# Optimization experiments

Measured on AMD Instinct MI355X. Metric: run time of the kernel, lower is better.

The kernel has to match this reference:

```python
import jax, jax.numpy as jnp
import numpy as np
from jax import lax

GAMMA = 0.001  # init kwarg gamma
DN = ('NCHW', 'OIHW', 'NCHW')


def _maxpool2(x):
    # 2x2 max pool, stride 2, NCHW
    return lax.reduce_window(x, -jnp.inf, lax.max, (1, 1, 2, 2), (1, 1, 2, 2), 'VALID')


def _features(x, w1, b1, w2, b2):
    h = lax.conv_general_dilated(x, w1, (1, 1), 'SAME', dimension_numbers=DN)
    h = _maxpool2(jax.nn.relu(h + b1[None, :, None, None]))
    h = lax.conv_general_dilated(h, w2, (1, 1), 'SAME', dimension_numbers=DN)
    h = _maxpool2(jax.nn.relu(h + b2[None, :, None, None]))
    return h.reshape(h.shape[0], -1)  # [N, 16*7*7=784]


def setup_inputs() -> dict:
    key = jax.random.key(0)
    ks = jax.random.split(key, 7)
    x = jax.random.normal(ks[0], (4096, 1, 28, 28), dtype=jnp.float32)
    w1 = jax.random.normal(ks[1], (8, 1, 3, 3), dtype=jnp.float32) * 0.1
    b1 = jax.random.normal(ks[2], (8,), dtype=jnp.float32) * 0.1
    w2 = jax.random.normal(ks[3], (16, 8, 3, 3), dtype=jnp.float32) * 0.1
    b2 = jax.random.normal(ks[4], (16,), dtype=jnp.float32) * 0.1
    support = jax.random.uniform(ks[5], (8192, 784), dtype=jnp.float32)
    alpha = jax.random.normal(ks[6], (8192, 4), dtype=jnp.float32)
    return {'x': x, 'w1': w1, 'b1': b1, 'w2': w2, 'b2': b2,
            'support': support, 'alpha': alpha}


def reference(x, w1, b1, w2, b2, support, alpha):
    feats = _features(x, w1, b1, w2, b2)                      # [N, 784]
    # Pairwise squared distances via expansion (replaces the N*M python loop)
    f2 = jnp.sum(feats * feats, axis=1, keepdims=True)        # [N, 1]
    s2 = jnp.sum(support * support, axis=1)[None, :]          # [1, M]
    d2 = f2 + s2 - 2.0 * (feats @ support.T)                  # [N, M]
    K = jnp.exp(-GAMMA * d2)                                  # RBF kernel matrix
    return K @ alpha                                          # [N, n_classes]
```

## Files before the change

kernel.cpp:

```cpp
#include <hip/hip_runtime.h>
#include <hip/hip_bf16.h>
#include <cstdint>

#define GAMMA 0.001f
#define TILE_BYTES 114688

typedef __attribute__((ext_vector_type(4))) float f32x4;
typedef __attribute__((ext_vector_type(8))) int v8i;
typedef __attribute__((ext_vector_type(8))) short bh8;
typedef unsigned char u8;

__device__ inline unsigned pack4_fp8(float4 f) {
  unsigned p = __builtin_amdgcn_cvt_pk_fp8_f32(f.x, f.y, 0, false);
  p = __builtin_amdgcn_cvt_pk_fp8_f32(f.z, f.w, p, true);
  return p;
}

__device__ inline ushort bf16u(float v) {
  __hip_bfloat16 h = __float2bfloat16(v);
  return *(ushort*)&h;
}

__global__ __launch_bounds__(256, 4) void conv_prep_kernel(
    const float* __restrict__ x, const float* __restrict__ w1,
    const float* __restrict__ b1, const float* __restrict__ w2,
    const float* __restrict__ b2, const float* __restrict__ support,
    const float* __restrict__ alpha, u8* __restrict__ feats_t,
    u8* __restrict__ sup_t, float* __restrict__ beta,
    float* __restrict__ ef) {
  int tid = threadIdx.x;
  int bx = blockIdx.x;

  if (bx >= 2048) {
    int lane = tid & 63, wave = tid >> 6;
    int m = (bx - 2048) * 4 + wave;
    const float* row = support + (size_t)m * 784;
    int mt = m >> 7, mr = m & 127;
    u8* tb = sup_t + (size_t)mt * TILE_BYTES;
    float ss = 0.f;
    if (lane < 56) {
      uint4 w;
      if (lane < 49) {
        float4 f0 = ((const float4*)row)[lane * 4 + 0];
        float4 f1 = ((const float4*)row)[lane * 4 + 1];
        float4 f2 = ((const float4*)row)[lane * 4 + 2];
        float4 f3 = ((const float4*)row)[lane * 4 + 3];
        ss = f0.x * f0.x + f0.y * f0.y + f0.z * f0.z + f0.w * f0.w +
             f1.x * f1.x + f1.y * f1.y + f1.z * f1.z + f1.w * f1.w +
             f2.x * f2.x + f2.y * f2.y + f2.z * f2.z + f2.w * f2.w +
             f3.x * f3.x + f3.y * f3.y + f3.z * f3.z + f3.w * f3.w;
        w.x = pack4_fp8(f0); w.y = pack4_fp8(f1);
        w.z = pack4_fp8(f2); w.w = pack4_fp8(f3);
      } else {
        w.x = 0; w.y = 0; w.z = 0; w.w = 0;
      }
      int kk = lane >> 3, u = lane & 7, q = u >> 1, h = u & 1;
      int qs = q ^ ((mr >> 1) & 3);
      *(uint4*)(tb + kk * 16384 + h * 8192 + mr * 64 + qs * 16) = w;
    }
#pragma unroll
    for (int s = 1; s < 64; s <<= 1) ss += __shfl_xor(ss, s, 64);
    if (lane == 0) {
      float es = __expf(-GAMMA * ss);
      float4 a = ((const float4*)alpha)[m];
      float4 b;
      b.x = es * a.x; b.y = es * a.y; b.z = es * a.z; b.w = es * a.w;
      ((float4*)beta)[m] = b;
    }
    return;
  }

  __shared__ float xp[2][900];
  __shared__ alignas(16) ushort a1h[2][2048];
  __shared__ float w1s[72], b1s[8], b2s[16];
  __shared__ float w2s[1152];
  __shared__ alignas(8) ushort sc[2][16][212];
  __shared__ alignas(16) u8 fb[2][784];
  __shared__ float red[256];

  int lane = tid & 63, wave = tid >> 6;

  for (int t = tid; t < 1800; t += 256) ((float*)xp)[t] = 0.f;
  for (int t = tid; t < 1024; t += 256) ((uint4*)a1h)[t] = (uint4){0, 0, 0, 0};
  if (tid < 72) w1s[tid] = w1[tid];
  if (tid < 8) b1s[tid] = b1[tid];
  if (tid < 16) b2s[tid] = b2[tid];
  for (int t = tid; t < 1152; t += 256) w2s[t] = w2[t];
  __syncthreads();

  int oc = lane & 15, quad = lane >> 4;
  bh8 wf[3];
#pragma unroll
  for (int g = 0; g < 3; g++) {
    int tap = g * 4 + quad;
#pragma unroll
    for (int j = 0; j < 8; j++) {
      float v = (tap < 9) ? w2s[oc * 72 + j * 9 + tap] : 0.f;
      wf[g][j] = (short)bf16u(v);
    }
  }

  for (int t = tid; t < 392; t += 256) {
    int img = t >= 196, j = t - img * 196;
    float4 v = ((const float4*)(x + (size_t)(bx * 2 + img) * 784))[j];
    int r = j / 7, c = (j % 7) * 4;
    float* p = &xp[img][(r + 1) * 30 + (c + 1)];
    p[0] = v.x; p[1] = v.y; p[2] = v.z; p[3] = v.w;
  }
  __syncthreads();

  for (int idx = tid; idx < 3136; idx += 256) {
    int img = idx >= 1568;
    int rem = idx - img * 1568;
    int c = rem / 196, r2 = rem % 196;
    int ph = r2 / 14, pw = r2 % 14;
    const float* w = &w1s[c * 9];
    const float* xb = &xp[img][(2 * ph) * 30 + (2 * pw)];
    float t[4][4];
#pragma unroll
    for (int a = 0; a < 4; a++) {
      float2 u0 = *(const float2*)(xb + a * 30);
      float2 u1 = *(const float2*)(xb + a * 30 + 2);
      t[a][0] = u0.x; t[a][1] = u0.y; t[a][2] = u1.x; t[a][3] = u1.y;
    }
    float s00 = 0, s01 = 0, s10 = 0, s11 = 0;
#pragma unroll
    for (int dy = 0; dy < 3; dy++)
#pragma unroll
      for (int dx = 0; dx < 3; dx++) {
        float wv = w[dy * 3 + dx];
        s00 += t[dy][dx] * wv;     s01 += t[dy][dx + 1] * wv;
        s10 += t[dy + 1][dx] * wv; s11 += t[dy + 1][dx + 1] * wv;
      }
    float mx = fmaxf(fmaxf(s00, s01), fmaxf(s10, s11));
    float val = fmaxf(mx + b1s[c], 0.f);
    a1h[img][((ph + 1) * 16 + (pw + 1)) * 8 + c] = bf16u(val);
  }
  __syncthreads();

  {
    int img2 = wave >> 1, half = wave & 1;
    int Tstart = half * 7, Tcnt = half ? 6 : 7;
    const ushort* abase = a1h[img2];
    int mrow = lane & 15;
    for (int t = 0; t < Tcnt; ++t) {
      int T = Tstart + t;
      int p = T * 16 + mrow;
      int pc = p > 195 ? 195 : p;
      int y = pc / 14, xq = pc - y * 14;
      int cell = y * 16 + xq;
      f32x4 acc = (f32x4){0, 0, 0, 0};
#pragma unroll
      for (int g = 0; g < 3; g++) {
        int tap = g * 4 + quad;
        const ushort* ap;
        if (g == 2 && quad > 0) {
          ap = abase;
        } else {
          int dy = tap / 3, dx = tap - dy * 3;
          ap = abase + (cell + dy * 16 + dx) * 8;
        }
        bh8 af = *(const bh8*)ap;
        acc = __builtin_amdgcn_mfma_f32_16x16x32_bf16(af, wf[g], acc, 0, 0, 0);
      }
      int pos0 = T * 16 + quad * 4;
      ushort4 s4;
      s4.x = bf16u(acc.x); s4.y = bf16u(acc.y);
      s4.z = bf16u(acc.z); s4.w = bf16u(acc.w);
      *(ushort4*)(&sc[img2][oc][pos0]) = s4;
    }
  }
  __syncthreads();

  int img = tid >> 7, r = tid & 127;
  float fsq = 0.f;
  if (r < 112) {
    int o = r & 15, y7 = r >> 4;
    const ushort* srow = sc[img][o];
    float bo = b2s[o];
#pragma unroll
    for (int x7 = 0; x7 < 7; x7++) {
      int p = 28 * y7 + 2 * x7;
      unsigned u0 = *(const unsigned*)(&srow[p]);
      unsigned u1 = *(const unsigned*)(&srow[p + 14]);
      float a = __uint_as_float(u0 << 16);
      float b = __uint_as_float(u0 & 0xffff0000u);
      float c = __uint_as_float(u1 << 16);
      float d = __uint_as_float(u1 & 0xffff0000u);
      float mx = fmaxf(fmaxf(a, b), fmaxf(c, d));
      float val = fmaxf(mx + bo, 0.f);
      fb[img][o * 49 + y7 * 7 + x7] =
          (u8)(__builtin_amdgcn_cvt_pk_fp8_f32(val, 0.f, 0, false) & 0xff);
      fsq += val * val;
    }
  }
  red[tid] = fsq;
  __syncthreads();
  for (int s = 64; s > 0; s >>= 1) {
    if ((tid & 127) < s) red[tid] += red[tid + s];
    __syncthreads();
  }
  if ((tid & 127) == 0) ef[bx * 2 + img] = __expf(-GAMMA * red[tid]);

  if (tid < 112) {
    int im = tid >= 56, j = tid - im * 56;
    uint4 v;
    if (j < 49) v = ((const uint4*)fb[im])[j];
    else { v.x = 0; v.y = 0; v.z = 0; v.w = 0; }
    int n = bx * 2 + im;
    int nt = n >> 7, nr = n & 127;
    int kk = j >> 3, u = j & 7, q = u >> 1, h = u & 1;
    int qs = q ^ ((nr >> 1) & 3);
    *(uint4*)(feats_t + (size_t)nt * TILE_BYTES + kk * 16384 + h * 8192 +
              nr * 64 + qs * 16) = v;
  }
}

__global__ __launch_bounds__(256, 2) void rbf_gemm_kernel(
    const u8* __restrict__ feats_t, const u8* __restrict__ sup_t,
    const float* __restrict__ beta, float* __restrict__ partial) {
  __shared__ alignas(16) u8 As[16384];
  __shared__ alignas(16) u8 Bs[16384];
  int tid = threadIdx.x;
  int wave = tid >> 6, lane = tid & 63;
  int bx = blockIdx.x;
  int chunk = bx & 63, nb = bx >> 6;
  const u8* at = feats_t + (size_t)nb * TILE_BYTES;
  const u8* bt = sup_t + (size_t)chunk * TILE_BYTES;
  int wn = wave >> 1, wm = wave & 1;
  int col = lane & 15, quad = lane >> 4;
  int slot = quad ^ ((col >> 1) & 3);

  f32x4 acc[4][4];
#pragma unroll
  for (int i = 0; i < 4; i++)
#pragma unroll
    for (int j = 0; j < 4; j++) acc[i][j] = (f32x4){0, 0, 0, 0};

  for (int kk = 0; kk < 7; ++kk) {
    const u8* ak = at + kk * 16384 + tid * 16;
    const u8* bk = bt + kk * 16384 + tid * 16;
    u8* la = As + tid * 16;
    u8* lb = Bs + tid * 16;
#pragma unroll
    for (int s = 0; s < 4; s++) {
      __builtin_amdgcn_global_load_lds(
          (const __attribute__((address_space(1))) void*)(ak + s * 4096),
          (__attribute__((address_space(3))) void*)(la + s * 4096), 16, 0, 0);
      __builtin_amdgcn_global_load_lds(
          (const __attribute__((address_space(1))) void*)(bk + s * 4096),
          (__attribute__((address_space(3))) void*)(lb + s * 4096), 16, 0, 0);
    }
    __syncthreads();
    v8i av[4], bv[4];
#pragma unroll
    for (int i = 0; i < 4; i++) {
      const u8* p = As + (wn * 64 + i * 16 + col) * 64 + slot * 16;
      int4 lo = *(const int4*)p;
      int4 hi = *(const int4*)(p + 8192);
      av[i] = (v8i){lo.x, lo.y, lo.z, lo.w, hi.x, hi.y, hi.z, hi.w};
    }
#pragma unroll
    for (int j = 0; j < 4; j++) {
      const u8* p = Bs + (wm * 64 + j * 16 + col) * 64 + slot * 16;
      int4 lo = *(const int4*)p;
      int4 hi = *(const int4*)(p + 8192);
      bv[j] = (v8i){lo.x, lo.y, lo.z, lo.w, hi.x, hi.y, hi.z, hi.w};
    }
#pragma unroll
    for (int i = 0; i < 4; i++)
#pragma unroll
      for (int j = 0; j < 4; j++)
        acc[i][j] = __builtin_amdgcn_mfma_scale_f32_16x16x128_f8f6f4(
            av[i], bv[j], acc[i][j], 0, 0, 0, 0x7f7f7f7f, 0, 0x7f7f7f7f);
    __syncthreads();
  }

#pragma unroll
  for (int i = 0; i < 4; i++)
#pragma unroll
    for (int j = 0; j < 4; j++) {
      acc[i][j].x = __expf(2.f * GAMMA * acc[i][j].x);
      acc[i][j].y = __expf(2.f * GAMMA * acc[i][j].y);
      acc[i][j].z = __expf(2.f * GAMMA * acc[i][j].z);
      acc[i][j].w = __expf(2.f * GAMMA * acc[i][j].w);
    }
  int n0 = nb * 128, m0 = chunk * 128;
#pragma unroll
  for (int c = 0; c < 4; ++c) {
    float bl[4];
#pragma unroll
    for (int j = 0; j < 4; j++)
      bl[j] = beta[(m0 + wm * 64 + j * 16 + col) * 4 + c];
#pragma unroll
    for (int i = 0; i < 4; i++) {
      f32x4 s = acc[i][0] * bl[0] + acc[i][1] * bl[1] + acc[i][2] * bl[2] +
                acc[i][3] * bl[3];
#pragma unroll
      for (int st = 1; st < 16; st <<= 1) {
        s.x += __shfl_xor(s.x, st, 16);
        s.y += __shfl_xor(s.y, st, 16);
        s.z += __shfl_xor(s.z, st, 16);
        s.w += __shfl_xor(s.w, st, 16);
      }
      if (col == c) {
        int n = n0 + wn * 64 + i * 16 + quad * 4;
        float* pp = partial + (((size_t)chunk * 2 + wm) * 4096 + n) * 4 + c;
        pp[0] = s.x; pp[4] = s.y; pp[8] = s.z; pp[12] = s.w;
      }
    }
  }
}

__global__ __launch_bounds__(256) void reduce_kernel(
    const float* __restrict__ partial, const float* __restrict__ ef,
    float* __restrict__ out) {
  __shared__ float4 sred[4][64];
  int nl = threadIdx.x & 63, chq = threadIdx.x >> 6;
  int n = blockIdx.x * 64 + nl;
  const float4* p = (const float4*)partial;
  float sx = 0, sy = 0, sz = 0, sw = 0;
  for (int ch = chq * 32; ch < chq * 32 + 32; ch++) {
    float4 v = p[(size_t)ch * 4096 + n];
    sx += v.x; sy += v.y; sz += v.z; sw += v.w;
  }
  sred[chq][nl] = (float4){sx, sy, sz, sw};
  __syncthreads();
  if (chq == 0) {
    float4 a = sred[0][nl], b = sred[1][nl], c = sred[2][nl], d = sred[3][nl];
    float e = ef[n];
    float4 o;
    o.x = e * (a.x + b.x + c.x + d.x);
    o.y = e * (a.y + b.y + c.y + d.y);
    o.z = e * (a.z + b.z + c.z + d.z);
    o.w = e * (a.w + b.w + c.w + d.w);
    ((float4*)out)[n] = o;
  }
}

extern "C" void kernel_launch(void* const* d_in, const int* in_sizes, int n_in,
                              void* d_out, int out_size, void* d_ws,
                              size_t ws_size, hipStream_t stream) {
  const float* x = (const float*)d_in[0];
  const float* w1 = (const float*)d_in[1];
  const float* b1 = (const float*)d_in[2];
  const float* w2 = (const float*)d_in[3];
  const float* b2 = (const float*)d_in[4];
  const float* support = (const float*)d_in[5];
  const float* alpha = (const float*)d_in[6];
  float* out = (float*)d_out;

  u8* ws = (u8*)d_ws;
  u8* sup_t = ws;
  u8* feats_t = ws + 7340032;
  float* beta = (float*)(ws + 11010048);
  float* ef = (float*)(ws + 11141120);
  float* partial = (float*)(ws + 11157504);

  conv_prep_kernel<<<4096, 256, 0, stream>>>(x, w1, b1, w2, b2, support, alpha,
                                             feats_t, sup_t, beta, ef);
  rbf_gemm_kernel<<<2048, 256, 0, stream>>>(feats_t, sup_t, beta, partial);
  reduce_kernel<<<64, 256, 0, stream>>>(partial, ef, out);
}
```

Baseline: 167.8 us.

## Load GEMM operand fragments directly from global memory, dropping LDS staging

The RBF GEMM kernel no longer stages A and B tiles through shared memory with global_load_lds and barriers. Each wave now reads its MFMA fragments directly from the pre-swizzled global layout into registers, and the k-loop is unrolled by two. This removes the LDS round trip and both __syncthreads per iteration. In exchange, two waves sharing a tile each load the same data from global memory, so the kernel leans on L2/L1 hits and more register-held loads are in flight.

```diff
diff --git a/kernel.cpp b/kernel.cpp
--- a/kernel.cpp
+++ b/kernel.cpp
@@ -219,50 +219,40 @@
 __global__ __launch_bounds__(256, 2) void rbf_gemm_kernel(
     const u8* __restrict__ feats_t, const u8* __restrict__ sup_t,
     const float* __restrict__ beta, float* __restrict__ partial) {
-  __shared__ alignas(16) u8 As[16384];
-  __shared__ alignas(16) u8 Bs[16384];
   int tid = threadIdx.x;
   int wave = tid >> 6, lane = tid & 63;
   int bx = blockIdx.x;
   int chunk = bx & 63, nb = bx >> 6;
-  const u8* at = feats_t + (size_t)nb * TILE_BYTES;
-  const u8* bt = sup_t + (size_t)chunk * TILE_BYTES;
   int wn = wave >> 1, wm = wave & 1;
   int col = lane & 15, quad = lane >> 4;
   int slot = quad ^ ((col >> 1) & 3);
 
+  const u8* abase = feats_t + (size_t)nb * TILE_BYTES +
+                    (wn * 64 + col) * 64 + slot * 16;
+  const u8* bbase = sup_t + (size_t)chunk * TILE_BYTES +
+                    (wm * 64 + col) * 64 + slot * 16;
+
   f32x4 acc[4][4];
 #pragma unroll
   for (int i = 0; i < 4; i++)
 #pragma unroll
     for (int j = 0; j < 4; j++) acc[i][j] = (f32x4){0, 0, 0, 0};
 
+#pragma unroll 2
   for (int kk = 0; kk < 7; ++kk) {
-    const u8* ak = at + kk * 16384 + tid * 16;
-    const u8* bk = bt + kk * 16384 + tid * 16;
-    u8* la = As + tid * 16;
-    u8* lb = Bs + tid * 16;
-#pragma unroll
-    for (int s = 0; s < 4; s++) {
-      __builtin_amdgcn_global_load_lds(
-          (const __attribute__((address_space(1))) void*)(ak + s * 4096),
-          (__attribute__((address_space(3))) void*)(la + s * 4096), 16, 0, 0);
-      __builtin_amdgcn_global_load_lds(
-          (const __attribute__((address_space(1))) void*)(bk + s * 4096),
-          (__attribute__((address_space(3))) void*)(lb + s * 4096), 16, 0, 0);
-    }
-    __syncthreads();
+    const u8* ak = abase + kk * 16384;
+    const u8* bk = bbase + kk * 16384;
     v8i av[4], bv[4];
 #pragma unroll
     for (int i = 0; i < 4; i++) {
-      const u8* p = As + (wn * 64 + i * 16 + col) * 64 + slot * 16;
+      const u8* p = ak + i * 1024;
       int4 lo = *(const int4*)p;
       int4 hi = *(const int4*)(p + 8192);
       av[i] = (v8i){lo.x, lo.y, lo.z, lo.w, hi.x, hi.y, hi.z, hi.w};
     }
 #pragma unroll
     for (int j = 0; j < 4; j++) {
-      const u8* p = Bs + (wm * 64 + j * 16 + col) * 64 + slot * 16;
+      const u8* p = bk + j * 1024;
       int4 lo = *(const int4*)p;
       int4 hi = *(const int4*)(p + 8192);
       bv[j] = (v8i){lo.x, lo.y, lo.z, lo.w, hi.x, hi.y, hi.z, hi.w};
@@ -273,7 +263,6 @@
       for (int j = 0; j < 4; j++)
         acc[i][j] = __builtin_amdgcn_mfma_scale_f32_16x16x128_f8f6f4(
             av[i], bv[j], acc[i][j], 0, 0, 0, 0x7f7f7f7f, 0, 0x7f7f7f7f);
-    __syncthreads();
   }
 
 #pragma unroll
```

Result: slower. 172.0 us (+2.5%).
